# Performance work log

Hardware: AMD Instinct MI355X
Metric: run time of the kernel (lower is better)

## Reference

```python
import jax, jax.numpy as jnp
import numpy as np

B, S, HID = 2, 2048, 2048
NH, NKV, D = 32, 8, 64
G = NH // NKV  # kv groups


def rotate_half(x):
    x1, x2 = jnp.split(x, 2, axis=-1)
    return jnp.concatenate([-x2, x1], axis=-1)


def setup_inputs() -> dict:
    key = jax.random.key(0)
    ks = jax.random.split(key, 6)
    hidden_states = jax.random.normal(ks[0], (B, S, HID), dtype=jnp.float32)
    # rotary tables [S, D]
    inv_freq = 1.0 / (10000.0 ** (jnp.arange(0, D, 2, dtype=jnp.float32) / D))
    t = jnp.arange(S, dtype=jnp.float32)
    freqs = jnp.einsum('s,d->sd', t, inv_freq)
    emb = jnp.concatenate([freqs, freqs], axis=-1)
    cos, sin = jnp.cos(emb), jnp.sin(emb)
    # additive causal mask [B,1,S,S]
    causal = jnp.triu(jnp.full((S, S), -1e9, dtype=jnp.float32), k=1)
    attention_mask = jnp.broadcast_to(causal, (B, 1, S, S))
    sc = 0.02
    wq = jax.random.normal(ks[1], (HID, 2 * NH * D), dtype=jnp.float32) * sc
    wk = jax.random.normal(ks[2], (HID, NKV * D), dtype=jnp.float32) * sc
    wv = jax.random.normal(ks[3], (HID, NKV * D), dtype=jnp.float32) * sc
    wo = jax.random.normal(ks[4], (HID, HID), dtype=jnp.float32) * sc
    return {"hidden_states": hidden_states, "cos": cos, "sin": sin,
            "attention_mask": attention_mask, "wq": wq, "wk": wk, "wv": wv, "wo": wo}


def reference(hidden_states, cos, sin, attention_mask, wq, wk, wv, wo):
    b, s, _ = hidden_states.shape
    qg = hidden_states @ wq                      # [B,S,2*NH*D]
    q, gate = jnp.split(qg, 2, axis=-1)
    q = q.reshape(b, s, NH, D).transpose(0, 2, 1, 3)        # [B,NH,S,D]
    k = (hidden_states @ wk).reshape(b, s, NKV, D).transpose(0, 2, 1, 3)
    v = (hidden_states @ wv).reshape(b, s, NKV, D).transpose(0, 2, 1, 3)  # computed, unused (as in source)
    # RoPE (cos/sin broadcast over batch and heads)
    c = cos[None, None]; sn = sin[None, None]
    q = q * c + rotate_half(q) * sn
    k = k * c + rotate_half(k) * sn
    # GQA repeat_kv
    k = jnp.repeat(k, G, axis=1)                 # [B,NH,S,D]
    # no 1/sqrt(d) scaling in source
    attn = jnp.einsum('bhqd,bhkd->bhqk', q, k) + attention_mask
    w = jax.nn.softmax(attn.astype(jnp.float32), axis=-1).astype(q.dtype)
    # NOTE: source multiplies weights by key_states (not value_states) — reproduced faithfully
    out = jnp.einsum('bhqk,bhkd->bhqd', w, k)
    out = out.transpose(0, 2, 1, 3).reshape(b, s, HID)
    out = out * jax.nn.sigmoid(gate)
    return out @ wo
```

## Files before the change

kernel.cpp:

```cpp
#include <hip/hip_runtime.h>

typedef float f32x4 __attribute__((ext_vector_type(4)));
typedef short bf16x8 __attribute__((ext_vector_type(8)));

__device__ __forceinline__ float bf2f(unsigned short h) {
  return __uint_as_float(((unsigned int)h) << 16);
}
__device__ __forceinline__ unsigned short f2bf(float f) {
  unsigned int u = __float_as_uint(f);
  unsigned int r = u + 0x7fffu + ((u >> 16) & 1u);
  return (unsigned short)(r >> 16);
}
__device__ __forceinline__ float fast_exp2(float x) {
  return __builtin_amdgcn_exp2f(x);
}
__device__ __forceinline__ unsigned cvt_pk_bf16(float lo, float hi) {
  unsigned d;
  asm("v_cvt_pk_bf16_f32 %0, %1, %2" : "=v"(d) : "v"(lo), "v"(hi));
  return d;
}
__device__ __forceinline__ float max3f(float a, float b, float c) {
  float d;
  asm("v_max3_f32 %0, %1, %2, %3" : "=v"(d) : "v"(a), "v"(b), "v"(c));
  return d;
}

__device__ __forceinline__ void gload_lds16(const void* g, void* l) {
  __builtin_amdgcn_global_load_lds((const __attribute__((address_space(1))) void*)g,
                                   (__attribute__((address_space(3))) void*)l, 16, 0, 0);
}

__global__ void conv_bf16(const float* __restrict__ src, unsigned short* __restrict__ dst, int n4) {
  for (int i = blockIdx.x * blockDim.x + threadIdx.x; i < n4; i += gridDim.x * blockDim.x) {
    float4 v = ((const float4*)src)[i];
    ushort4 o;
    o.x = f2bf(v.x); o.y = f2bf(v.y); o.z = f2bf(v.z); o.w = f2bf(v.w);
    ((ushort4*)dst)[i] = o;
  }
}

__global__ void tconv(const float* __restrict__ src, unsigned short* __restrict__ dst,
                      int C, int dstRowOff, int dstLD) {
  __shared__ float tile[32][33];
  int c0 = blockIdx.x * 32, r0 = blockIdx.y * 32;
  int tx = threadIdx.x, ty = threadIdx.y;
#pragma unroll
  for (int i = 0; i < 4; ++i)
    tile[ty + i * 8][tx] = src[(size_t)(r0 + ty + i * 8) * C + c0 + tx];
  __syncthreads();
#pragma unroll
  for (int i = 0; i < 4; ++i)
    dst[(size_t)(dstRowOff + c0 + ty + i * 8) * dstLD + r0 + tx] = f2bf(tile[tx][ty + i * 8]);
}

template <typename OutT>
__global__ __launch_bounds__(256) void gemm_bt(const unsigned short* __restrict__ A,
                                               const unsigned short* __restrict__ BT,
                                               OutT* __restrict__ C, int M, int N, int K) {
  __shared__ unsigned short As[128 * 64];
  __shared__ unsigned short Bs[128 * 64];
  const int tid = threadIdx.x;
  const int lane = tid & 63;
  const int wid = tid >> 6;
  const int g = lane >> 4, l15 = lane & 15;
  const int wr = wid >> 1, wc = wid & 1;
  const int bm = blockIdx.y, bn = blockIdx.x;
  const unsigned short* Ab = A + (size_t)bm * 128 * K;
  const unsigned short* Bb = BT + (size_t)bn * 128 * K;
  f32x4 acc[4][4] = {};
  int Rj[4], csj[4];
#pragma unroll
  for (int j = 0; j < 4; ++j) {
    int c = j * 256 + tid;
    Rj[j] = c >> 3;
    csj[j] = ((c & 7) ^ (Rj[j] & 7)) * 8;
  }
  for (int k0 = 0; k0 < K; k0 += 64) {
#pragma unroll
    for (int j = 0; j < 4; ++j) {
      gload_lds16(Ab + (size_t)Rj[j] * K + k0 + csj[j], &As[(j * 256 + (wid << 6)) * 8]);
      gload_lds16(Bb + (size_t)Rj[j] * K + k0 + csj[j], &Bs[(j * 256 + (wid << 6)) * 8]);
    }
    __syncthreads();
    bf16x8 af[4][2], bfr[4][2];
#pragma unroll
    for (int i = 0; i < 4; ++i)
#pragma unroll
      for (int kk = 0; kk < 2; ++kk) {
        int rowa = wr * 64 + i * 16 + l15;
        int cha = ((kk * 4 + g) ^ (rowa & 7)) * 8;
        af[i][kk] = *(const bf16x8*)&As[rowa * 64 + cha];
        int rowb = wc * 64 + i * 16 + l15;
        int chb = ((kk * 4 + g) ^ (rowb & 7)) * 8;
        bfr[i][kk] = *(const bf16x8*)&Bs[rowb * 64 + chb];
      }
    __builtin_amdgcn_s_setprio(1);
#pragma unroll
    for (int kk = 0; kk < 2; ++kk)
#pragma unroll
      for (int i = 0; i < 4; ++i)
#pragma unroll
        for (int j = 0; j < 4; ++j)
          acc[i][j] = __builtin_amdgcn_mfma_f32_16x16x32_bf16(af[i][kk], bfr[j][kk], acc[i][j], 0, 0, 0);
    __builtin_amdgcn_s_setprio(0);
    __syncthreads();
  }
  const int rbase = bm * 128 + wr * 64 + ((lane >> 4) << 2);
  const int cbase = bn * 128 + wc * 64 + l15;
#pragma unroll
  for (int i = 0; i < 4; ++i)
#pragma unroll
    for (int j = 0; j < 4; ++j)
#pragma unroll
      for (int r = 0; r < 4; ++r) {
        int row = rbase + i * 16 + r;
        int col = cbase + j * 16;
        if constexpr (sizeof(OutT) == 2)
          C[(size_t)row * N + col] = f2bf(acc[i][j][r]);
        else
          C[(size_t)row * N + col] = acc[i][j][r];
      }
}

__global__ __launch_bounds__(256) void gemm_qgk(const unsigned short* __restrict__ A,
                                                const unsigned short* __restrict__ BT,
                                                const float* __restrict__ cosT,
                                                const float* __restrict__ sinT,
                                                unsigned short* __restrict__ qrope,
                                                unsigned short* __restrict__ gateb,
                                                unsigned short* __restrict__ krope,
                                                unsigned short* __restrict__ kT) {
  const int K = 2048;
  __shared__ unsigned short As[128 * 64];
  __shared__ unsigned short Bs[128 * 64];
  const int tid = threadIdx.x;
  const int lane = tid & 63;
  const int wid = tid >> 6;
  const int g = lane >> 4, l15 = lane & 15;
  const int wr = wid >> 1, wc = wid & 1;
  const int bm = blockIdx.y, bn = blockIdx.x;
  const unsigned short* Ab = A + (size_t)bm * 128 * K;
  const unsigned short* Bb = BT + (size_t)bn * 128 * K;
  f32x4 acc[4][4] = {};
  int Rj[4], csj[4];
#pragma unroll
  for (int j = 0; j < 4; ++j) {
    int c = j * 256 + tid;
    Rj[j] = c >> 3;
    csj[j] = ((c & 7) ^ (Rj[j] & 7)) * 8;
  }
  for (int k0 = 0; k0 < K; k0 += 64) {
#pragma unroll
    for (int j = 0; j < 4; ++j) {
      gload_lds16(Ab + (size_t)Rj[j] * K + k0 + csj[j], &As[(j * 256 + (wid << 6)) * 8]);
      gload_lds16(Bb + (size_t)Rj[j] * K + k0 + csj[j], &Bs[(j * 256 + (wid << 6)) * 8]);
    }
    __syncthreads();
    bf16x8 af[4][2], bfr[4][2];
#pragma unroll
    for (int i = 0; i < 4; ++i)
#pragma unroll
      for (int kk = 0; kk < 2; ++kk) {
        int rowa = wr * 64 + i * 16 + l15;
        int cha = ((kk * 4 + g) ^ (rowa & 7)) * 8;
        af[i][kk] = *(const bf16x8*)&As[rowa * 64 + cha];
        int rowb = wc * 64 + i * 16 + l15;
        int chb = ((kk * 4 + g) ^ (rowb & 7)) * 8;
        bfr[i][kk] = *(const bf16x8*)&Bs[rowb * 64 + chb];
      }
    __builtin_amdgcn_s_setprio(1);
#pragma unroll
    for (int kk = 0; kk < 2; ++kk)
#pragma unroll
      for (int i = 0; i < 4; ++i)
#pragma unroll
        for (int j = 0; j < 4; ++j)
          acc[i][j] = __builtin_amdgcn_mfma_f32_16x16x32_bf16(af[i][kk], bfr[j][kk], acc[i][j], 0, 0, 0);
    __builtin_amdgcn_s_setprio(0);
    __syncthreads();
  }
  const int rbase = bm * 128 + wr * 64 + ((lane >> 4) << 2);
  if (bn < 16) {
    const int h = bn * 2 + wc;
#pragma unroll
    for (int i = 0; i < 4; ++i)
#pragma unroll
      for (int j = 0; j < 4; ++j)
#pragma unroll
        for (int r = 0; r < 4; ++r) {
          int row = rbase + i * 16 + r;
          int b = row >> 11, s = row & 2047;
          int d = j * 16 + l15;
          float c = cosT[s * 64 + d], sn = sinT[s * 64 + d];
          float x = acc[i][j][r], xp = acc[i][j ^ 2][r];
          float v = x * c + (((j & 2) == 0) ? -xp : xp) * sn;
          qrope[((size_t)(b * 32 + h) * 2048 + s) * 64 + d] = f2bf(v * 1.44269504089f);
        }
  } else if (bn < 32) {
    const int cb = (bn - 16) * 128 + wc * 64;
#pragma unroll
    for (int i = 0; i < 4; ++i)
#pragma unroll
      for (int j = 0; j < 4; ++j)
#pragma unroll
        for (int r = 0; r < 4; ++r) {
          int row = rbase + i * 16 + r;
          int b = row >> 11, s = row & 2047;
          gateb[(size_t)(b * 2048 + s) * 2048 + cb + j * 16 + l15] = f2bf(acc[i][j][r]);
        }
  } else {
    const int kh = (bn - 32) * 2 + wc;
#pragma unroll
    for (int i = 0; i < 4; ++i)
#pragma unroll
      for (int j = 0; j < 4; ++j)
#pragma unroll
        for (int r = 0; r < 4; ++r) {
          int row = rbase + i * 16 + r;
          int b = row >> 11, s = row & 2047;
          int d = j * 16 + l15;
          float c = cosT[s * 64 + d], sn = sinT[s * 64 + d];
          float x = acc[i][j][r], xp = acc[i][j ^ 2][r];
          float v = x * c + (((j & 2) == 0) ? -xp : xp) * sn;
          unsigned short bv = f2bf(v);
          krope[((size_t)(b * 8 + kh) * 2048 + s) * 64 + d] = bv;
          kT[((size_t)(b * 8 + kh) * 64 + d) * 2048 + s] = bv;
        }
  }
}

__global__ __launch_bounds__(256) void attn_fused(const unsigned short* __restrict__ qrope,
                                                  const unsigned short* __restrict__ krope,
                                                  const unsigned short* __restrict__ kT,
                                                  const unsigned short* __restrict__ gateb,
                                                  unsigned short* __restrict__ attng) {
  __shared__ unsigned short Ks[2][64 * 64];
  __shared__ unsigned short KTs[2][64 * 64];
  __shared__ unsigned short Ps[128 * 64];
  const int qblk = 15 - blockIdx.y;
  const int bh = blockIdx.x;
  const int b = bh >> 5, h = bh & 31, kh = h >> 2;
  const int q0 = qblk * 128;
  const int tid = threadIdx.x, lane = tid & 63, wid = tid >> 6;
  const int g = lane >> 4, l15 = lane & 15;
  const unsigned short* Qbase = qrope + ((size_t)(b * 32 + h) * 2048 + q0) * 64;
  const unsigned short* Kbase = krope + (size_t)(b * 8 + kh) * 2048 * 64;
  const unsigned short* KTbase = kT + (size_t)(b * 8 + kh) * 64 * 2048;

#pragma unroll
  for (int j = 0; j < 2; ++j) {
    int F = ((j * 4 + wid) << 10) + (lane << 4);
    int R = F >> 7;
    int cs = ((F >> 4) & 7) ^ (R & 7);
    gload_lds16(Kbase + (size_t)R * 64 + cs * 8, &Ks[0][(j * 4 + wid) << 9]);
    gload_lds16(KTbase + (size_t)R * 2048 + cs * 8, &KTs[0][(j * 4 + wid) << 9]);
  }
  bf16x8 qf[2][2];
#pragma unroll
  for (int i = 0; i < 2; ++i)
#pragma unroll
    for (int ks = 0; ks < 2; ++ks)
      qf[i][ks] = *(const bf16x8*)(Qbase + (size_t)(wid * 32 + i * 16 + l15) * 64 + ks * 32 + g * 8);
  __syncthreads();

  f32x4 oaccT[2][4] = {};
  float mrow[2] = {-1e30f, -1e30f}, lrow[2] = {0.f, 0.f};

  const int nt = 2 * qblk + 2;
  for (int t = 0; t < nt; ++t) {
    const int cur = t & 1;
    if (t + 1 < nt) {
      const int nb = cur ^ 1;
#pragma unroll
      for (int j = 0; j < 2; ++j) {
        int F = ((j * 4 + wid) << 10) + (lane << 4);
        int R = F >> 7;
        int cs = ((F >> 4) & 7) ^ (R & 7);
        gload_lds16(Kbase + (size_t)((t + 1) * 64 + R) * 64 + cs * 8, &Ks[nb][(j * 4 + wid) << 9]);
        gload_lds16(KTbase + (size_t)R * 2048 + (t + 1) * 64 + cs * 8, &KTs[nb][(j * 4 + wid) << 9]);
      }
    }
    f32x4 st[2][4] = {};
#pragma unroll
    for (int ks = 0; ks < 2; ++ks) {
      bf16x8 kf[4];
#pragma unroll
      for (int nf = 0; nf < 4; ++nf) {
        int row = nf * 16 + l15;
        int ch = (ks * 4 + g) ^ (row & 7);
        kf[nf] = *(const bf16x8*)&Ks[cur][row * 64 + ch * 8];
      }
      __builtin_amdgcn_s_setprio(1);
#pragma unroll
      for (int i = 0; i < 2; ++i)
#pragma unroll
        for (int nf = 0; nf < 4; ++nf)
          st[i][nf] = __builtin_amdgcn_mfma_f32_16x16x32_bf16(kf[nf], qf[i][ks], st[i][nf], 0, 0, 0);
      __builtin_amdgcn_s_setprio(0);
    }
    if (t >= 2 * qblk) {
#pragma unroll
      for (int i = 0; i < 2; ++i) {
        int qabs = q0 + wid * 32 + i * 16 + l15;
#pragma unroll
        for (int nf = 0; nf < 4; ++nf)
#pragma unroll
          for (int r = 0; r < 4; ++r) {
            int kabs = t * 64 + nf * 16 + 4 * g + r;
            if (kabs > qabs) st[i][nf][r] += -1e9f;
          }
      }
    }
#pragma unroll
    for (int i = 0; i < 2; ++i) {
      float a0 = max3f(st[i][0][0], st[i][0][1], st[i][0][2]);
      float a1 = max3f(st[i][0][3], st[i][1][0], st[i][1][1]);
      float a2 = max3f(st[i][1][2], st[i][1][3], st[i][2][0]);
      float a3 = max3f(st[i][2][1], st[i][2][2], st[i][2][3]);
      float a4 = max3f(st[i][3][0], st[i][3][1], st[i][3][2]);
      float pm = fmaxf(max3f(a0, a1, a2), max3f(a3, a4, st[i][3][3]));
      pm = fmaxf(pm, __shfl_xor(pm, 16, 64));
      pm = fmaxf(pm, __shfl_xor(pm, 32, 64));
      if (!__all(pm <= mrow[i] + 8.f)) {
        float mnew = fmaxf(mrow[i], pm);
        float scale = fast_exp2(mrow[i] - mnew);
        mrow[i] = mnew;
        lrow[i] *= scale;
#pragma unroll
        for (int df = 0; df < 4; ++df)
#pragma unroll
          for (int r = 0; r < 4; ++r) oaccT[i][df][r] *= scale;
      }
      float rs = 0.f;
#pragma unroll
      for (int nf = 0; nf < 4; ++nf)
#pragma unroll
        for (int r = 0; r < 4; ++r) {
          float p = fast_exp2(st[i][nf][r] - mrow[i]);
          st[i][nf][r] = p;
          rs += p;
        }
      rs += __shfl_xor(rs, 16, 64);
      rs += __shfl_xor(rs, 32, 64);
      lrow[i] += rs;
    }
#pragma unroll
    for (int i = 0; i < 2; ++i) {
      int q = wid * 32 + i * 16 + l15;
#pragma unroll
      for (int nf = 0; nf < 4; ++nf) {
        int k0 = nf * 16 + 4 * g;
        int ch = (k0 >> 3) ^ (q & 7);
        unsigned w0 = cvt_pk_bf16(st[i][nf][0], st[i][nf][1]);
        unsigned w1 = cvt_pk_bf16(st[i][nf][2], st[i][nf][3]);
        *(uint2*)&Ps[q * 64 + ch * 8 + (k0 & 7)] = make_uint2(w0, w1);
      }
    }
#pragma unroll
    for (int ks = 0; ks < 2; ++ks) {
      bf16x8 pf[2], vf[4];
#pragma unroll
      for (int i = 0; i < 2; ++i) {
        int row = wid * 32 + i * 16 + l15;
        int ch = (ks * 4 + g) ^ (row & 7);
        pf[i] = *(const bf16x8*)&Ps[row * 64 + ch * 8];
      }
#pragma unroll
      for (int df = 0; df < 4; ++df) {
        int row = df * 16 + l15;
        int ch = (ks * 4 + g) ^ (row & 7);
        vf[df] = *(const bf16x8*)&KTs[cur][row * 64 + ch * 8];
      }
      __builtin_amdgcn_s_setprio(1);
#pragma unroll
      for (int i = 0; i < 2; ++i)
#pragma unroll
        for (int df = 0; df < 4; ++df)
          oaccT[i][df] = __builtin_amdgcn_mfma_f32_16x16x32_bf16(vf[df], pf[i], oaccT[i][df], 0, 0, 0);
      __builtin_amdgcn_s_setprio(0);
    }
    __syncthreads();
  }
#pragma unroll
  for (int i = 0; i < 2; ++i) {
    float rl = 1.f / lrow[i];
    int qabs = q0 + wid * 32 + i * 16 + l15;
    size_t grow = (size_t)b * 2048 + qabs;
#pragma unroll
    for (int df = 0; df < 4; ++df) {
      int d0 = df * 16 + 4 * g;
      ushort4 gt = *(const ushort4*)&gateb[grow * 2048 + h * 64 + d0];
      float o0 = oaccT[i][df][0] * rl * (1.f / (1.f + __expf(-bf2f(gt.x))));
      float o1 = oaccT[i][df][1] * rl * (1.f / (1.f + __expf(-bf2f(gt.y))));
      float o2 = oaccT[i][df][2] * rl * (1.f / (1.f + __expf(-bf2f(gt.z))));
      float o3 = oaccT[i][df][3] * rl * (1.f / (1.f + __expf(-bf2f(gt.w))));
      *(uint2*)&attng[grow * 2048 + h * 64 + d0] =
          make_uint2(cvt_pk_bf16(o0, o1), cvt_pk_bf16(o2, o3));
    }
  }
}

extern "C" void kernel_launch(void* const* d_in, const int* in_sizes, int n_in,
                              void* d_out, int out_size, void* d_ws, size_t ws_size,
                              hipStream_t stream) {
  const float* hidden = (const float*)d_in[0];
  const float* cosT = (const float*)d_in[1];
  const float* sinT = (const float*)d_in[2];
  const float* wq = (const float*)d_in[4];
  const float* wk = (const float*)d_in[5];
  const float* wo = (const float*)d_in[7];
  char* ws = (char*)d_ws;
  unsigned short* hb16  = (unsigned short*)(ws + 0);
  unsigned short* wcatT = (unsigned short*)(ws + 16777216);
  unsigned short* woT   = (unsigned short*)(ws + 35651584);
  unsigned short* gateb = (unsigned short*)(ws + 44040192);
  unsigned short* qrope = (unsigned short*)(ws + 60817408);
  unsigned short* krope = (unsigned short*)(ws + 77594624);
  unsigned short* kTb   = (unsigned short*)(ws + 81788928);
  unsigned short* attng = (unsigned short*)(ws + 85983232);

  conv_bf16<<<dim3(2048), dim3(256), 0, stream>>>(hidden, hb16, 2097152);
  tconv<<<dim3(128, 64), dim3(32, 8), 0, stream>>>(wq, wcatT, 4096, 0, 2048);
  tconv<<<dim3(16, 64), dim3(32, 8), 0, stream>>>(wk, wcatT, 512, 4096, 2048);
  tconv<<<dim3(64, 64), dim3(32, 8), 0, stream>>>(wo, woT, 2048, 0, 2048);
  gemm_qgk<<<dim3(36, 32), dim3(256), 0, stream>>>(hb16, wcatT, cosT, sinT,
                                                   qrope, gateb, krope, kTb);
  attn_fused<<<dim3(64, 16), dim3(256), 0, stream>>>(qrope, krope, kTb, gateb, attng);
  gemm_bt<float><<<dim3(16, 32), dim3(256), 0, stream>>>(attng, woT, (float*)d_out, 4096, 2048, 2048);
}
```

Measured before the change: 306.1 us.

## Move K transpose to separate kernel, read V fragments directly, reorder attention blocks

Drops the scattered transposed-K writes from the QGK GEMM epilogue and adds a separate LDS-tiled ktrans kernel that builds kT. Inside attention, the transposed-K fragments now come straight from global memory into registers instead of being staged through a double-buffered LDS tile, which saves LDS space. The attention grid becomes 1D, with a block mapping that interleaves long and short causal query blocks and groups heads for balance and L2 locality. The costs are an extra kernel launch and global-latency loads in the inner loop that are no longer prefetched.

```diff
diff --git a/kernel.cpp b/kernel.cpp
--- a/kernel.cpp
+++ b/kernel.cpp
@@ -128,8 +128,7 @@
                                                 const float* __restrict__ sinT,
                                                 unsigned short* __restrict__ qrope,
                                                 unsigned short* __restrict__ gateb,
-                                                unsigned short* __restrict__ krope,
-                                                unsigned short* __restrict__ kT) {
+                                                unsigned short* __restrict__ krope) {
   const int K = 2048;
   __shared__ unsigned short As[128 * 64];
   __shared__ unsigned short Bs[128 * 64];
@@ -222,11 +221,25 @@
           float c = cosT[s * 64 + d], sn = sinT[s * 64 + d];
           float x = acc[i][j][r], xp = acc[i][j ^ 2][r];
           float v = x * c + (((j & 2) == 0) ? -xp : xp) * sn;
-          unsigned short bv = f2bf(v);
-          krope[((size_t)(b * 8 + kh) * 2048 + s) * 64 + d] = bv;
-          kT[((size_t)(b * 8 + kh) * 64 + d) * 2048 + s] = bv;
+          krope[((size_t)(b * 8 + kh) * 2048 + s) * 64 + d] = f2bf(v);
         }
   }
+}
+
+__global__ void ktrans(const unsigned short* __restrict__ krope, unsigned short* __restrict__ kT) {
+  __shared__ unsigned short tile[64][65];
+  int bh = blockIdx.y;
+  int s0 = blockIdx.x * 64;
+  const unsigned short* src = krope + (size_t)bh * 2048 * 64;
+  unsigned short* dst = kT + (size_t)bh * 64 * 2048;
+  int tx = threadIdx.x & 63, ty = threadIdx.x >> 6;
+#pragma unroll
+  for (int i = 0; i < 16; ++i)
+    tile[ty + i * 4][tx] = src[(size_t)(s0 + ty + i * 4) * 64 + tx];
+  __syncthreads();
+#pragma unroll
+  for (int i = 0; i < 16; ++i)
+    dst[(size_t)(ty + i * 4) * 2048 + s0 + tx] = tile[tx][ty + i * 4];
 }
 
 __global__ __launch_bounds__(256) void attn_fused(const unsigned short* __restrict__ qrope,
@@ -235,10 +248,11 @@
                                                   const unsigned short* __restrict__ gateb,
                                                   unsigned short* __restrict__ attng) {
   __shared__ unsigned short Ks[2][64 * 64];
-  __shared__ unsigned short KTs[2][64 * 64];
   __shared__ unsigned short Ps[128 * 64];
-  const int qblk = 15 - blockIdx.y;
-  const int bh = blockIdx.x;
+  const int id = blockIdx.x;
+  const int bh = (id & 7) | ((id >> 7) << 3);
+  const int q2 = (id >> 3) & 15;
+  const int qblk = (q2 & 1) ? (q2 >> 1) : 15 - (q2 >> 1);
   const int b = bh >> 5, h = bh & 31, kh = h >> 2;
   const int q0 = qblk * 128;
   const int tid = threadIdx.x, lane = tid & 63, wid = tid >> 6;
@@ -253,7 +267,6 @@
     int R = F >> 7;
     int cs = ((F >> 4) & 7) ^ (R & 7);
     gload_lds16(Kbase + (size_t)R * 64 + cs * 8, &Ks[0][(j * 4 + wid) << 9]);
-    gload_lds16(KTbase + (size_t)R * 2048 + cs * 8, &KTs[0][(j * 4 + wid) << 9]);
   }
   bf16x8 qf[2][2];
 #pragma unroll
@@ -277,9 +290,14 @@
         int R = F >> 7;
         int cs = ((F >> 4) & 7) ^ (R & 7);
         gload_lds16(Kbase + (size_t)((t + 1) * 64 + R) * 64 + cs * 8, &Ks[nb][(j * 4 + wid) << 9]);
-        gload_lds16(KTbase + (size_t)R * 2048 + (t + 1) * 64 + cs * 8, &KTs[nb][(j * 4 + wid) << 9]);
-      }
-    }
+      }
+    }
+    bf16x8 vf[2][4];
+#pragma unroll
+    for (int ks = 0; ks < 2; ++ks)
+#pragma unroll
+      for (int df = 0; df < 4; ++df)
+        vf[ks][df] = *(const bf16x8*)(KTbase + (size_t)(df * 16 + l15) * 2048 + t * 64 + ks * 32 + g * 8);
     f32x4 st[2][4] = {};
 #pragma unroll
     for (int ks = 0; ks < 2; ++ks) {
@@ -358,25 +376,19 @@
     }
 #pragma unroll
     for (int ks = 0; ks < 2; ++ks) {
-      bf16x8 pf[2], vf[4];
+      bf16x8 pf[2];
 #pragma unroll
       for (int i = 0; i < 2; ++i) {
         int row = wid * 32 + i * 16 + l15;
         int ch = (ks * 4 + g) ^ (row & 7);
         pf[i] = *(const bf16x8*)&Ps[row * 64 + ch * 8];
       }
-#pragma unroll
-      for (int df = 0; df < 4; ++df) {
-        int row = df * 16 + l15;
-        int ch = (ks * 4 + g) ^ (row & 7);
-        vf[df] = *(const bf16x8*)&KTs[cur][row * 64 + ch * 8];
-      }
       __builtin_amdgcn_s_setprio(1);
 #pragma unroll
       for (int i = 0; i < 2; ++i)
 #pragma unroll
         for (int df = 0; df < 4; ++df)
-          oaccT[i][df] = __builtin_amdgcn_mfma_f32_16x16x32_bf16(vf[df], pf[i], oaccT[i][df], 0, 0, 0);
+          oaccT[i][df] = __builtin_amdgcn_mfma_f32_16x16x32_bf16(vf[ks][df], pf[i], oaccT[i][df], 0, 0, 0);
       __builtin_amdgcn_s_setprio(0);
     }
     __syncthreads();
@@ -424,7 +436,8 @@
   tconv<<<dim3(16, 64), dim3(32, 8), 0, stream>>>(wk, wcatT, 512, 4096, 2048);
   tconv<<<dim3(64, 64), dim3(32, 8), 0, stream>>>(wo, woT, 2048, 0, 2048);
   gemm_qgk<<<dim3(36, 32), dim3(256), 0, stream>>>(hb16, wcatT, cosT, sinT,
-                                                   qrope, gateb, krope, kTb);
-  attn_fused<<<dim3(64, 16), dim3(256), 0, stream>>>(qrope, krope, kTb, gateb, attng);
+                                                   qrope, gateb, krope);
+  ktrans<<<dim3(32, 16), dim3(256), 0, stream>>>(krope, kTb);
+  attn_fused<<<dim3(1024), dim3(256), 0, stream>>>(qrope, krope, kTb, gateb, attng);
   gemm_bt<float><<<dim3(16, 32), dim3(256), 0, stream>>>(attng, woT, (float*)d_out, 4096, 2048, 2048);
 }
```

Result: slower. 320.0 us (+4.6%).
